# Kernel optimization log

Measured on AMD Instinct MI355X. Metric: run time of the kernel, lower is better.

## Reference

```python
import jax, jax.numpy as jnp
import numpy as np

B, N, D, H = 4, 1024, 256, 8  # batch, seq, in_dim(=per-head qkv_dim), n_heads


def setup_inputs() -> dict:
    key = jax.random.key(0)
    k1, k2, k3 = jax.random.split(key, 3)
    x = jax.random.normal(k1, (B, N, D), dtype=jnp.float32)
    Wqkv = jax.random.normal(k2, (D, 3 * D * H), dtype=jnp.float32) * 0.02
    bqkv = jnp.zeros((3 * D * H,), dtype=jnp.float32)
    W0 = jax.random.normal(k3, (D * H, D), dtype=jnp.float32) * 0.02
    b0 = jnp.zeros((D,), dtype=jnp.float32)
    return {"x": x, "Wqkv": Wqkv, "bqkv": bqkv, "W0": W0, "b0": b0}


def reference(x, Wqkv, bqkv, W0, b0):
    b, n, d = x.shape
    h = Wqkv.shape[1] // (3 * d)
    qkv = x @ Wqkv + bqkv                      # [b, n, 3*d*h]
    # Faithful to torch: raw row-major reinterpretation of the buffer.
    q, k, v = jnp.reshape(qkv, (3, b, n, d, h))
    score = jnp.einsum('bnqh,btqh->bnth', q, k) * (d ** -0.5)  # [b, n, n, h]
    attn = jax.nn.softmax(score, axis=1)       # softmax over query axis (dim=1), as in source
    # einsum 'bnnh,bnqh->bnqh' = diagonal of attn times v (faithful to source)
    av = jnp.einsum('bnnh,bnqh->bnqh', attn, v)  # [b, n, d, h]
    out = av.reshape(b, n, d * h) @ W0 + b0    # [b, n, d]
    return out
```

## Files before the change

### kernel.cpp

```cpp
#include <hip/hip_runtime.h>


#define SEGSZ 8388608

typedef short v8s __attribute__((ext_vector_type(8)));
typedef float v4f __attribute__((ext_vector_type(4)));

__device__ __forceinline__ ushort f2bf(float v) {
  union { float f; unsigned u; } x; x.f = v;
  const unsigned r = x.u + 0x7fff + ((x.u >> 16) & 1);
  return (ushort)(r >> 16);
}
__device__ __forceinline__ float bf2f(ushort v) {
  union { unsigned u; float f; } x; x.u = ((unsigned)v) << 16;
  return x.f;
}

#define GLOAD_LDS16(g, l)                                            \
  __builtin_amdgcn_global_load_lds(                                  \
      (const __attribute__((address_space(1))) void*)(g),            \
      (__attribute__((address_space(3))) void*)(l), 16, 0, 0)

__global__ __launch_bounds__(256) void prep(
    const float* __restrict__ X, const float* __restrict__ Wqkv,
    const float* __restrict__ W0, ushort* __restrict__ xb,
    ushort* __restrict__ whT, ushort* __restrict__ w0T) {
  __shared__ float T[64][65];
  const int tid = threadIdx.x;
  int bid = blockIdx.x;

  if (bid < 1024) {
    const size_t i = ((size_t)bid * 256 + tid) * 4;
    const float4 v = *(const float4*)&X[i];
    ushort4 hv = {f2bf(v.x), f2bf(v.y), f2bf(v.z), f2bf(v.w)};
    *(ushort4*)&xb[i] = hv;
    return;
  }
  bid -= 1024;
  if (bid < 384) {
    const int n0 = (bid % 96) * 64;
    const int k0 = (bid / 96) * 64;
    {
      const int row = tid >> 2;
      const int c0 = (tid & 3) * 16;
#pragma unroll
      for (int j = 0; j < 16; j += 4) {
        const float4 v = *(const float4*)&Wqkv[(size_t)(k0 + row) * 6144 + n0 + c0 + j];
        T[row][c0 + j + 0] = v.x; T[row][c0 + j + 1] = v.y;
        T[row][c0 + j + 2] = v.z; T[row][c0 + j + 3] = v.w;
      }
    }
    __syncthreads();
    {
      const int nn = tid >> 2;
      const int kk0 = (tid & 3) * 16;
      const int n = n0 + nn;
      const int seg = n >> 11, h = n & 7, d = (n & 2047) >> 3;
      const int p = seg * 2048 + h * 256 + d;
      ushort hv[16];
#pragma unroll
      for (int j = 0; j < 16; ++j) hv[j] = f2bf(T[kk0 + j][nn]);
      const size_t base = (size_t)p * 256 + k0 + kk0;
#pragma unroll
      for (int j = 0; j < 16; j += 8) *(v8s*)&whT[base + j] = *(v8s*)&hv[j];
    }
    return;
  }
  bid -= 384;
  {
    const int e0 = (bid & 3) * 64;
    const int k0 = (bid >> 2) * 64;
    {
      const int row = tid >> 2;
      const int c0 = (tid & 3) * 16;
#pragma unroll
      for (int j = 0; j < 16; j += 4) {
        const float4 v = *(const float4*)&W0[(size_t)(k0 + row) * 256 + e0 + c0 + j];
        T[row][c0 + j + 0] = v.x; T[row][c0 + j + 1] = v.y;
        T[row][c0 + j + 2] = v.z; T[row][c0 + j + 3] = v.w;
      }
    }
    __syncthreads();
    {
      const int ee = tid >> 2;
      const int kk0 = (tid & 3) * 16;
#pragma unroll
      for (int j = 0; j < 16; ++j) {
        const int k = k0 + kk0 + j;
        const int d = k >> 3, h = k & 7;
        w0T[(size_t)(e0 + ee) * 2048 + h * 256 + d] = f2bf(T[kk0 + j][ee]);
      }
    }
  }
}

template <int STRIDE>
__device__ __forceinline__ void gemm128_k64(
    const ushort* __restrict__ gA, const ushort* __restrict__ gB,
    ushort (&AS)[8192], ushort (&BS)[8192], v4f (&acc)[4][4]) {
  const int tid = threadIdx.x;
  const int wave = tid >> 6, lane = tid & 63;
  const int quad = lane >> 4, l15 = lane & 15;
  const int wr = (wave >> 1) * 64;
  const int wc = (wave & 1) * 64;
  const int srow = lane >> 3;
  const int scol = (((lane & 7) ^ srow) << 3);

#pragma unroll
  for (int kt = 0; kt < 4; ++kt) {
#pragma unroll
    for (int j = 0; j < 4; ++j) {
      const size_t grow =
          (size_t)(j * 32 + wave * 8 + srow) * STRIDE + kt * 64 + scol;
      GLOAD_LDS16(gA + grow, &AS[j * 2048 + wave * 512]);
      GLOAD_LDS16(gB + grow, &BS[j * 2048 + wave * 512]);
    }
    __syncthreads();
#pragma unroll
    for (int ks = 0; ks < 2; ++ks) {
      v8s aF[4], bF[4];
      const int rx = l15 & 7;
#pragma unroll
      for (int i = 0; i < 4; ++i) {
        aF[i] = *(const v8s*)&AS[(wr + i * 16 + l15) * 64 +
                                 ((((ks << 2) | quad) ^ rx) << 3)];
        bF[i] = *(const v8s*)&BS[(wc + i * 16 + l15) * 64 +
                                 ((((ks << 2) | quad) ^ rx) << 3)];
      }
#pragma unroll
      for (int ri = 0; ri < 4; ++ri)
#pragma unroll
        for (int ci = 0; ci < 4; ++ci)
          acc[ri][ci] = __builtin_amdgcn_mfma_f32_16x16x32_bf16(
              aF[ri], bF[ci], acc[ri][ci], 0, 0, 0);
    }
    __syncthreads();
  }
}

__global__ __launch_bounds__(256) void qkv_mfma(
    const ushort* __restrict__ xb, const ushort* __restrict__ whT,
    const float* __restrict__ bias, ushort* __restrict__ qkvb) {
  __shared__ ushort As[8192];
  __shared__ ushort Bh[8192];
  const int tid = threadIdx.x;
  const int wave = tid >> 6, lane = tid & 63;
  const int quad = lane >> 4, l15 = lane & 15;
  const int c0 = blockIdx.x * 128;
  const int r0 = blockIdx.y * 128;
  const int wr = (wave >> 1) * 64;
  const int wc = (wave & 1) * 64;

  v4f acc[4][4] = {};
  gemm128_k64<256>(xb + (size_t)r0 * 256, whT + (size_t)c0 * 256, As, Bh, acc);

#pragma unroll
  for (int ci = 0; ci < 4; ++ci) {
    const int c = c0 + wc + ci * 16 + l15;
    const int cseg = c >> 11;
    const int h = (c & 2047) >> 8;
    const int d = c & 255;
    const float bv = bias[cseg * 2048 + d * 8 + h];
#pragma unroll
    for (int ri = 0; ri < 4; ++ri)
#pragma unroll
      for (int rg = 0; rg < 4; ++rg) {
        const int r = r0 + wr + ri * 16 + quad * 4 + rg;
        const int g = r * 3 + cseg;
        const int seg = g >> 12;
        const int tok = g & 4095;
        float val = acc[ri][ci][rg] + bv;
        if (seg == 0) val *= 0.0625f;
        qkvb[(size_t)seg * SEGSZ + (size_t)tok * 2048 + h * 256 + d] = f2bf(val);
      }
  }
}

__global__ __launch_bounds__(256) void mid_fused(
    const ushort* __restrict__ qkvb, const ushort* __restrict__ w0T,
    float* __restrict__ pl, float* __restrict__ sd_ws,
    ushort* __restrict__ partial) {
  __shared__ ushort S1[8192];
  __shared__ ushort S2[8192];
  __shared__ float redL[2][2][64];

  const int tid = threadIdx.x;
  const int wave = tid >> 6, lane = tid & 63;
  const int quad = lane >> 4, l15 = lane & 15;
  const int wr = (wave >> 1) * 64;
  const int wc = (wave & 1) * 64;
  const int id = blockIdx.x;

  v4f acc[4][4] = {};

  if (id < 2048) {
    const int bh = (id >> 9) * 8 + (id & 7);
    const int tile = (id >> 3) & 63;
    const int tt0 = (tile >> 3) * 128;
    const int nn0 = (tile & 7) * 128;
    const int b = bh >> 3, h = bh & 7;
    const ushort* Qg = qkvb + (size_t)b * 1024 * 2048 + h * 256;
    const ushort* Kg = Qg + SEGSZ;

    gemm128_k64<2048>(Qg + (size_t)nn0 * 2048, Kg + (size_t)tt0 * 2048,
                      S1, S2, acc);

    float lsum[4];
#pragma unroll
    for (int ci = 0; ci < 4; ++ci) {
      float s = 0.f;
#pragma unroll
      for (int ri = 0; ri < 4; ++ri)
#pragma unroll
        for (int rg = 0; rg < 4; ++rg) s += __expf(acc[ri][ci][rg]);
      s += __shfl_xor(s, 16, 64);
      s += __shfl_xor(s, 32, 64);
      lsum[ci] = s;
    }
    if (quad == 0) {
#pragma unroll
      for (int ci = 0; ci < 4; ++ci)
        redL[wave & 1][wave >> 1][ci * 16 + l15] = lsum[ci];
    }
    __syncthreads();
    if ((wave >> 1) == 0 && quad == 0) {
#pragma unroll
      for (int ci = 0; ci < 4; ++ci) {
        const int t = tt0 + (wave & 1) * 64 + ci * 16 + l15;
        const float l = lsum[ci] + redL[wave & 1][1][ci * 16 + l15];
        pl[((size_t)bh * 1024 + t) * 8 + (tile & 7)] = l;
      }
    }

    if (tt0 == nn0 && (wave == 0 || wave == 3) && quad == (l15 >> 2)) {
#pragma unroll
      for (int ri = 0; ri < 4; ++ri) {
        const int t = tt0 + (wave & 1) * 64 + ri * 16 + l15;
        sd_ws[(size_t)bh * 1024 + t] = acc[ri][ri][l15 & 3];
      }
    }
  } else {
    const int j = id - 2048;
    const int e0 = (j & 1) * 128;
    const int tok0 = ((j >> 1) & 31) * 128;
    const int h = j >> 6;
    const ushort* vb = qkvb + 2 * (size_t)SEGSZ;

    gemm128_k64<2048>(vb + (size_t)tok0 * 2048 + h * 256,
                      w0T + (size_t)e0 * 2048 + h * 256, S1, S2, acc);

#pragma unroll
    for (int ri = 0; ri < 4; ++ri)
#pragma unroll
      for (int rg = 0; rg < 4; ++rg) {
        const int lrow = wr + ri * 16 + quad * 4 + rg;
        const int tok = tok0 + lrow;
#pragma unroll
        for (int ci = 0; ci < 4; ++ci) {
          const int e = e0 + wc + ci * 16 + l15;
          partial[(size_t)h * 1048576 + (size_t)tok * 256 + e] =
              f2bf(acc[ri][ci][rg]);
        }
      }
  }
}

__global__ __launch_bounds__(256) void av_atomic(
    const ushort* __restrict__ vb, const ushort* __restrict__ w0T,
    const float* __restrict__ pl, const float* __restrict__ sd,
    float* __restrict__ out) {
  __shared__ ushort As[8192];
  __shared__ ushort Bs[8192];
  __shared__ float diagS[128];
  const int tid = threadIdx.x;
  const int wave = tid >> 6, lane = tid & 63;
  const int quad = lane >> 4, l15 = lane & 15;
  const int e0 = blockIdx.x * 128;
  const int tok0 = blockIdx.y * 128;
  const int h = blockIdx.z;
  const int wr = (wave >> 1) * 64;
  const int wc = (wave & 1) * 64;

  if (tid < 128) {
    const int bh = (tok0 >> 10) * 8 + h;
    const int t = (tok0 & 1023) + tid;
    const size_t base = ((size_t)bh * 1024 + t) * 8;
    float l = 0.f;
#pragma unroll
    for (int c = 0; c < 8; ++c) l += pl[base + c];
    diagS[tid] = __expf(sd[(size_t)bh * 1024 + t]) / l;
  }
  __syncthreads();

  v4f acc[4][4] = {};
  gemm128_k64<2048>(vb + (size_t)tok0 * 2048 + h * 256,
                    w0T + (size_t)e0 * 2048 + h * 256, As, Bs, acc);

#pragma unroll
  for (int ri = 0; ri < 4; ++ri)
#pragma unroll
    for (int rg = 0; rg < 4; ++rg) {
      const int lrow = wr + ri * 16 + quad * 4 + rg;
      const int tok = tok0 + lrow;
      const float dg = diagS[lrow];
#pragma unroll
      for (int ci = 0; ci < 4; ++ci) {
        const int e = e0 + wc + ci * 16 + l15;
        atomicAdd(&out[(size_t)tok * 256 + e], acc[ri][ci][rg] * dg);
      }
    }
}

__global__ void init_out(const float* __restrict__ b0, float* __restrict__ out) {
  const int i = blockIdx.x * 256 + threadIdx.x;
  const int e0 = (i & 63) << 2;
  *(float4*)&out[(size_t)i * 4] = *(const float4*)&b0[e0];
}

__global__ void reduce_out(const ushort* __restrict__ partial,
                           const float* __restrict__ pl,
                           const float* __restrict__ sd,
                           const float* __restrict__ b0, float* __restrict__ out) {
  __shared__ float dgS[32];
  const int i = blockIdx.x * 256 + threadIdx.x;
  const int tbase = blockIdx.x * 4;
  if (threadIdx.x < 32) {
    const int tl = threadIdx.x >> 3, h = threadIdx.x & 7;
    const int tok = tbase + tl;
    const int bh = (tok >> 10) * 8 + h;
    const int t = tok & 1023;
    const size_t base = ((size_t)bh * 1024 + t) * 8;
    float l = 0.f;
#pragma unroll
    for (int c = 0; c < 8; ++c) l += pl[base + c];
    dgS[threadIdx.x] = __expf(sd[(size_t)bh * 1024 + t]) / l;
  }
  __syncthreads();
  const int tl = threadIdx.x >> 6;
  const int e0 = (i & 63) << 2;
  float4 a = *(const float4*)&b0[e0];
#pragma unroll
  for (int h = 0; h < 8; ++h) {
    const float dg = dgS[tl * 8 + h];
    const ushort4 p = *(const ushort4*)&partial[(size_t)h * 1048576 + (size_t)i * 4];
    a.x += dg * bf2f(p.x); a.y += dg * bf2f(p.y);
    a.z += dg * bf2f(p.z); a.w += dg * bf2f(p.w);
  }
  *(float4*)&out[(size_t)i * 4] = a;
}

extern "C" void kernel_launch(void* const* d_in, const int* in_sizes, int n_in,
                              void* d_out, int out_size, void* d_ws, size_t ws_size,
                              hipStream_t stream) {
  const float* x    = (const float*)d_in[0];
  const float* Wqkv = (const float*)d_in[1];
  const float* bqkv = (const float*)d_in[2];
  const float* W0   = (const float*)d_in[3];
  const float* b0   = (const float*)d_in[4];
  float* out = (float*)d_out;

  float*  pl   = (float*)d_ws;
  float*  sd   = pl + 262144;
  ushort* qkvb = (ushort*)(sd + 32768);
  ushort* xb   = qkvb + 3 * (size_t)SEGSZ;
  ushort* whT  = xb + 1048576;
  ushort* w0T  = whT + 1572864;
  ushort* partial = w0T + 524288;

  ushort* vb = qkvb + 2 * (size_t)SEGSZ;

  const size_t need_base =
      (size_t)(262144 + 32768) * 4 + (size_t)SEGSZ * 3 * 2 +
      (size_t)(1048576 + 1572864 + 524288) * 2;
  const bool full = ws_size >= need_base + (size_t)8 * 1048576 * 2;

  prep<<<1536, 256, 0, stream>>>(x, Wqkv, W0, xb, whT, w0T);
  qkv_mfma<<<dim3(48, 32), 256, 0, stream>>>(xb, whT, bqkv, qkvb);
  if (full) {
    mid_fused<<<2560, 256, 0, stream>>>(qkvb, w0T, pl, sd, partial);
    reduce_out<<<1024, 256, 0, stream>>>(partial, pl, sd, b0, out);
  } else {
    mid_fused<<<2048, 256, 0, stream>>>(qkvb, w0T, pl, sd, nullptr);
    init_out<<<1024, 256, 0, stream>>>(b0, out);
    av_atomic<<<dim3(2, 32, 8), 256, 0, stream>>>(vb, w0T, pl, sd, out);
  }
}
```

Measured before the change: 127.5 us.

## Double-buffer LDS tiles in shared GEMM helper to overlap loads with MFMA

Converts the 128x128xK256 GEMM helper to a two-stage LDS pipeline. It prefetches the next K-slice into the alternate buffer while MFMAs consume the current one, and uses explicit vmcnt waits with raw barriers. The goal is to hide global-to-LDS load latency behind compute. In exchange, LDS use per block doubles to 64KB across all three GEMM kernels, which may lower occupancy.

```diff
diff --git a/kernel.cpp b/kernel.cpp
--- a/kernel.cpp
+++ b/kernel.cpp
@@ -20,6 +20,10 @@
   __builtin_amdgcn_global_load_lds(                                  \
       (const __attribute__((address_space(1))) void*)(g),            \
       (__attribute__((address_space(3))) void*)(l), 16, 0, 0)
+
+#define SBAR()   __builtin_amdgcn_s_barrier()
+#define VMCNT8() asm volatile("s_waitcnt vmcnt(8)" ::: "memory")
+#define VMCNT0() asm volatile("s_waitcnt vmcnt(0)" ::: "memory")
 
 __global__ __launch_bounds__(256) void prep(
     const float* __restrict__ X, const float* __restrict__ Wqkv,
@@ -97,7 +101,7 @@
 template <int STRIDE>
 __device__ __forceinline__ void gemm128_k64(
     const ushort* __restrict__ gA, const ushort* __restrict__ gB,
-    ushort (&AS)[8192], ushort (&BS)[8192], v4f (&acc)[4][4]) {
+    ushort (&AS)[2][8192], ushort (&BS)[2][8192], v4f (&acc)[4][4]) {
   const int tid = threadIdx.x;
   const int wave = tid >> 6, lane = tid & 63;
   const int quad = lane >> 4, l15 = lane & 15;
@@ -106,26 +110,34 @@
   const int srow = lane >> 3;
   const int scol = (((lane & 7) ^ srow) << 3);
 
-#pragma unroll
-  for (int kt = 0; kt < 4; ++kt) {
+  auto stage = [&](int kt, int bi) {
 #pragma unroll
     for (int j = 0; j < 4; ++j) {
       const size_t grow =
           (size_t)(j * 32 + wave * 8 + srow) * STRIDE + kt * 64 + scol;
-      GLOAD_LDS16(gA + grow, &AS[j * 2048 + wave * 512]);
-      GLOAD_LDS16(gB + grow, &BS[j * 2048 + wave * 512]);
-    }
-    __syncthreads();
+      GLOAD_LDS16(gA + grow, &AS[bi][j * 2048 + wave * 512]);
+      GLOAD_LDS16(gB + grow, &BS[bi][j * 2048 + wave * 512]);
+    }
+  };
+
+  stage(0, 0);
+  stage(1, 1);
+  VMCNT8();
+  SBAR();
+
+#pragma unroll
+  for (int kt = 0; kt < 4; ++kt) {
+    const int cur = kt & 1;
 #pragma unroll
     for (int ks = 0; ks < 2; ++ks) {
       v8s aF[4], bF[4];
       const int rx = l15 & 7;
 #pragma unroll
       for (int i = 0; i < 4; ++i) {
-        aF[i] = *(const v8s*)&AS[(wr + i * 16 + l15) * 64 +
-                                 ((((ks << 2) | quad) ^ rx) << 3)];
-        bF[i] = *(const v8s*)&BS[(wc + i * 16 + l15) * 64 +
-                                 ((((ks << 2) | quad) ^ rx) << 3)];
+        aF[i] = *(const v8s*)&AS[cur][(wr + i * 16 + l15) * 64 +
+                                      ((((ks << 2) | quad) ^ rx) << 3)];
+        bF[i] = *(const v8s*)&BS[cur][(wc + i * 16 + l15) * 64 +
+                                      ((((ks << 2) | quad) ^ rx) << 3)];
       }
 #pragma unroll
       for (int ri = 0; ri < 4; ++ri)
@@ -134,15 +146,24 @@
           acc[ri][ci] = __builtin_amdgcn_mfma_f32_16x16x32_bf16(
               aF[ri], bF[ci], acc[ri][ci], 0, 0, 0);
     }
-    __syncthreads();
+    if (kt < 3) {
+      SBAR();
+      if (kt < 2) {
+        stage(kt + 2, cur);
+        VMCNT8();
+      } else {
+        VMCNT0();
+      }
+      SBAR();
+    }
   }
 }
 
 __global__ __launch_bounds__(256) void qkv_mfma(
     const ushort* __restrict__ xb, const ushort* __restrict__ whT,
     const float* __restrict__ bias, ushort* __restrict__ qkvb) {
-  __shared__ ushort As[8192];
-  __shared__ ushort Bh[8192];
+  __shared__ ushort As[2][8192];
+  __shared__ ushort Bh[2][8192];
   const int tid = threadIdx.x;
   const int wave = tid >> 6, lane = tid & 63;
   const int quad = lane >> 4, l15 = lane & 15;
@@ -180,8 +201,8 @@
     const ushort* __restrict__ qkvb, const ushort* __restrict__ w0T,
     float* __restrict__ pl, float* __restrict__ sd_ws,
     ushort* __restrict__ partial) {
-  __shared__ ushort S1[8192];
-  __shared__ ushort S2[8192];
+  __shared__ ushort S1[2][8192];
+  __shared__ ushort S2[2][8192];
   __shared__ float redL[2][2][64];
 
   const int tid = threadIdx.x;
@@ -269,8 +290,8 @@
     const ushort* __restrict__ vb, const ushort* __restrict__ w0T,
     const float* __restrict__ pl, const float* __restrict__ sd,
     float* __restrict__ out) {
-  __shared__ ushort As[8192];
-  __shared__ ushort Bs[8192];
+  __shared__ ushort As[2][8192];
+  __shared__ ushort Bs[2][8192];
   __shared__ float diagS[128];
   const int tid = threadIdx.x;
   const int wave = tid >> 6, lane = tid & 63;
```

After: 128.0 us. Within noise of the previous version (+0.4%).

## Load A operand directly into registers and stage only B through LDS

Applied to the files above, without the earlier changes.

The shared 128x128x256 GEMM helper now loads the A tile fragments straight from global memory into registers and stages only the B tile through LDS. K is processed in two halves of 128 instead of four steps of 64, and the swizzle is widened accordingly. This cuts LDS traffic and the number of barriers per GEMM. In exchange, A fragment loads are uncoalesced strided global reads, and holding 16 A fragments per half raises register pressure, which may lower occupancy.

```diff
diff --git a/kernel.cpp b/kernel.cpp
--- a/kernel.cpp
+++ b/kernel.cpp
@@ -20,6 +20,9 @@
   __builtin_amdgcn_global_load_lds(                                  \
       (const __attribute__((address_space(1))) void*)(g),            \
       (__attribute__((address_space(3))) void*)(l), 16, 0, 0)
+
+#define SBAR()   __builtin_amdgcn_s_barrier()
+#define VMCNT0() asm volatile("s_waitcnt vmcnt(0)" ::: "memory")
 
 __global__ __launch_bounds__(256) void prep(
     const float* __restrict__ X, const float* __restrict__ Wqkv,
@@ -95,54 +98,53 @@
 }
 
 template <int STRIDE>
-__device__ __forceinline__ void gemm128_k64(
+__device__ __forceinline__ void gemm128_breg(
     const ushort* __restrict__ gA, const ushort* __restrict__ gB,
-    ushort (&AS)[8192], ushort (&BS)[8192], v4f (&acc)[4][4]) {
+    ushort (&BS)[16384], v4f (&acc)[4][4]) {
   const int tid = threadIdx.x;
   const int wave = tid >> 6, lane = tid & 63;
   const int quad = lane >> 4, l15 = lane & 15;
   const int wr = (wave >> 1) * 64;
   const int wc = (wave & 1) * 64;
-  const int srow = lane >> 3;
-  const int scol = (((lane & 7) ^ srow) << 3);
-
-#pragma unroll
-  for (int kt = 0; kt < 4; ++kt) {
-#pragma unroll
-    for (int j = 0; j < 4; ++j) {
-      const size_t grow =
-          (size_t)(j * 32 + wave * 8 + srow) * STRIDE + kt * 64 + scol;
-      GLOAD_LDS16(gA + grow, &AS[j * 2048 + wave * 512]);
-      GLOAD_LDS16(gB + grow, &BS[j * 2048 + wave * 512]);
-    }
-    __syncthreads();
-#pragma unroll
-    for (int ks = 0; ks < 2; ++ks) {
-      v8s aF[4], bF[4];
-      const int rx = l15 & 7;
-#pragma unroll
-      for (int i = 0; i < 4; ++i) {
-        aF[i] = *(const v8s*)&AS[(wr + i * 16 + l15) * 64 +
-                                 ((((ks << 2) | quad) ^ rx) << 3)];
-        bF[i] = *(const v8s*)&BS[(wc + i * 16 + l15) * 64 +
-                                 ((((ks << 2) | quad) ^ rx) << 3)];
-      }
-#pragma unroll
-      for (int ri = 0; ri < 4; ++ri)
-#pragma unroll
-        for (int ci = 0; ci < 4; ++ci)
+  const int rlow = tid >> 4;
+  const int srccol = ((l15 ^ rlow) << 3);
+
+#pragma unroll
+  for (int half = 0; half < 2; ++half) {
+    if (half) SBAR();
+    v8s aF[4][4];
+#pragma unroll
+    for (int ri = 0; ri < 4; ++ri)
+#pragma unroll
+      for (int ks = 0; ks < 4; ++ks)
+        aF[ri][ks] = *(const v8s*)&gA[(size_t)(wr + ri * 16 + l15) * STRIDE +
+                                      half * 128 + ks * 32 + quad * 8];
+#pragma unroll
+    for (int j = 0; j < 8; ++j) {
+      GLOAD_LDS16(gB + (size_t)(j * 16 + rlow) * STRIDE + half * 128 + srccol,
+                  &BS[j * 2048 + wave * 512]);
+    }
+    VMCNT0();
+    SBAR();
+#pragma unroll
+    for (int ks = 0; ks < 4; ++ks) {
+#pragma unroll
+      for (int ci = 0; ci < 4; ++ci) {
+        const v8s bF = *(const v8s*)&BS[(wc + ci * 16 + l15) * 128 +
+                                        ((((ks << 2) | quad) ^ l15) << 3)];
+#pragma unroll
+        for (int ri = 0; ri < 4; ++ri)
           acc[ri][ci] = __builtin_amdgcn_mfma_f32_16x16x32_bf16(
-              aF[ri], bF[ci], acc[ri][ci], 0, 0, 0);
-    }
-    __syncthreads();
+              aF[ri][ks], bF, acc[ri][ci], 0, 0, 0);
+      }
+    }
   }
 }
 
 __global__ __launch_bounds__(256) void qkv_mfma(
     const ushort* __restrict__ xb, const ushort* __restrict__ whT,
     const float* __restrict__ bias, ushort* __restrict__ qkvb) {
-  __shared__ ushort As[8192];
-  __shared__ ushort Bh[8192];
+  __shared__ ushort Bs[16384];
   const int tid = threadIdx.x;
   const int wave = tid >> 6, lane = tid & 63;
   const int quad = lane >> 4, l15 = lane & 15;
@@ -152,7 +154,7 @@
   const int wc = (wave & 1) * 64;
 
   v4f acc[4][4] = {};
-  gemm128_k64<256>(xb + (size_t)r0 * 256, whT + (size_t)c0 * 256, As, Bh, acc);
+  gemm128_breg<256>(xb + (size_t)r0 * 256, whT + (size_t)c0 * 256, Bs, acc);
 
 #pragma unroll
   for (int ci = 0; ci < 4; ++ci) {
@@ -180,8 +182,7 @@
     const ushort* __restrict__ qkvb, const ushort* __restrict__ w0T,
     float* __restrict__ pl, float* __restrict__ sd_ws,
     ushort* __restrict__ partial) {
-  __shared__ ushort S1[8192];
-  __shared__ ushort S2[8192];
+  __shared__ ushort Bs[16384];
   __shared__ float redL[2][2][64];
 
   const int tid = threadIdx.x;
@@ -202,8 +203,8 @@
     const ushort* Qg = qkvb + (size_t)b * 1024 * 2048 + h * 256;
     const ushort* Kg = Qg + SEGSZ;
 
-    gemm128_k64<2048>(Qg + (size_t)nn0 * 2048, Kg + (size_t)tt0 * 2048,
-                      S1, S2, acc);
+    gemm128_breg<2048>(Qg + (size_t)nn0 * 2048, Kg + (size_t)tt0 * 2048,
+                       Bs, acc);
 
     float lsum[4];
 #pragma unroll
@@ -246,8 +247,8 @@
     const int h = j >> 6;
     const ushort* vb = qkvb + 2 * (size_t)SEGSZ;
 
-    gemm128_k64<2048>(vb + (size_t)tok0 * 2048 + h * 256,
-                      w0T + (size_t)e0 * 2048 + h * 256, S1, S2, acc);
+    gemm128_breg<2048>(vb + (size_t)tok0 * 2048 + h * 256,
+                       w0T + (size_t)e0 * 2048 + h * 256, Bs, acc);
 
 #pragma unroll
     for (int ri = 0; ri < 4; ++ri)
@@ -269,8 +270,7 @@
     const ushort* __restrict__ vb, const ushort* __restrict__ w0T,
     const float* __restrict__ pl, const float* __restrict__ sd,
     float* __restrict__ out) {
-  __shared__ ushort As[8192];
-  __shared__ ushort Bs[8192];
+  __shared__ ushort Bs[16384];
   __shared__ float diagS[128];
   const int tid = threadIdx.x;
   const int wave = tid >> 6, lane = tid & 63;
@@ -293,8 +293,8 @@
   __syncthreads();
 
   v4f acc[4][4] = {};
-  gemm128_k64<2048>(vb + (size_t)tok0 * 2048 + h * 256,
-                    w0T + (size_t)e0 * 2048 + h * 256, As, Bs, acc);
+  gemm128_breg<2048>(vb + (size_t)tok0 * 2048 + h * 256,
+                     w0T + (size_t)e0 * 2048 + h * 256, Bs, acc);
 
 #pragma unroll
   for (int ri = 0; ri < 4; ++ri)
```

After: 163.5 us. 1.28x slower.

## Store Q/K/V and W0T in contiguous 128x64 tile-blocked layout

Applied to the files above, without the earlier changes.

The QKV projection epilogue and the W0 transpose now write their bf16 outputs in a tiled layout. Each 128-row by 64-column K-slab is a contiguous 16 KB block, grouped per batch-head for Q/K and per head for V. The shared GEMM loader takes separate row and K strides, so the attention and V·W0 GEMMs read each k-tile from one contiguous region instead of rows strided by 2048 elements. The aim is better DRAM and TLB locality on the global-to-LDS loads, at the cost of more scattered, index-heavy stores in the QKV epilogue.

```diff
diff --git a/kernel.cpp b/kernel.cpp
--- a/kernel.cpp
+++ b/kernel.cpp
@@ -84,17 +84,19 @@
     {
       const int ee = tid >> 2;
       const int kk0 = (tid & 3) * 16;
+      const int e = e0 + ee;
 #pragma unroll
       for (int j = 0; j < 16; ++j) {
         const int k = k0 + kk0 + j;
         const int d = k >> 3, h = k & 7;
-        w0T[(size_t)(e0 + ee) * 2048 + h * 256 + d] = f2bf(T[kk0 + j][ee]);
-      }
-    }
-  }
-}
-
-template <int STRIDE>
+        w0T[(size_t)h * 65536 + (e >> 7) * 32768 + (d >> 6) * 8192 +
+            (e & 127) * 64 + (d & 63)] = f2bf(T[kk0 + j][ee]);
+      }
+    }
+  }
+}
+
+template <int RSTRIDE, int KSTRIDE>
 __device__ __forceinline__ void gemm128_k64(
     const ushort* __restrict__ gA, const ushort* __restrict__ gB,
     ushort (&AS)[8192], ushort (&BS)[8192], v4f (&acc)[4][4]) {
@@ -111,7 +113,7 @@
 #pragma unroll
     for (int j = 0; j < 4; ++j) {
       const size_t grow =
-          (size_t)(j * 32 + wave * 8 + srow) * STRIDE + kt * 64 + scol;
+          (size_t)(j * 32 + wave * 8 + srow) * RSTRIDE + kt * KSTRIDE + scol;
       GLOAD_LDS16(gA + grow, &AS[j * 2048 + wave * 512]);
       GLOAD_LDS16(gB + grow, &BS[j * 2048 + wave * 512]);
     }
@@ -152,7 +154,8 @@
   const int wc = (wave & 1) * 64;
 
   v4f acc[4][4] = {};
-  gemm128_k64<256>(xb + (size_t)r0 * 256, whT + (size_t)c0 * 256, As, Bh, acc);
+  gemm128_k64<256, 64>(xb + (size_t)r0 * 256, whT + (size_t)c0 * 256,
+                       As, Bh, acc);
 
 #pragma unroll
   for (int ci = 0; ci < 4; ++ci) {
@@ -171,7 +174,17 @@
         const int tok = g & 4095;
         float val = acc[ri][ci][rg] + bv;
         if (seg == 0) val *= 0.0625f;
-        qkvb[(size_t)seg * SEGSZ + (size_t)tok * 2048 + h * 256 + d] = f2bf(val);
+        size_t addr;
+        if (seg < 2) {
+          const int bh = (tok >> 10) * 8 + h;
+          const int t = tok & 1023;
+          addr = (size_t)seg * SEGSZ + (size_t)bh * 262144 +
+                 (t >> 7) * 32768 + (d >> 6) * 8192 + (t & 127) * 64 + (d & 63);
+        } else {
+          addr = 2 * (size_t)SEGSZ + (size_t)h * 1048576 +
+                 (tok >> 7) * 32768 + (d >> 6) * 8192 + (tok & 127) * 64 + (d & 63);
+        }
+        qkvb[addr] = f2bf(val);
       }
   }
 }
@@ -198,12 +211,10 @@
     const int tile = (id >> 3) & 63;
     const int tt0 = (tile >> 3) * 128;
     const int nn0 = (tile & 7) * 128;
-    const int b = bh >> 3, h = bh & 7;
-    const ushort* Qg = qkvb + (size_t)b * 1024 * 2048 + h * 256;
-    const ushort* Kg = Qg + SEGSZ;
-
-    gemm128_k64<2048>(Qg + (size_t)nn0 * 2048, Kg + (size_t)tt0 * 2048,
-                      S1, S2, acc);
+    const ushort* Qg = qkvb + (size_t)bh * 262144 + (nn0 >> 7) * 32768;
+    const ushort* Kg = qkvb + SEGSZ + (size_t)bh * 262144 + (tt0 >> 7) * 32768;
+
+    gemm128_k64<64, 8192>(Qg, Kg, S1, S2, acc);
 
     float lsum[4];
 #pragma unroll
@@ -244,10 +255,11 @@
     const int e0 = (j & 1) * 128;
     const int tok0 = ((j >> 1) & 31) * 128;
     const int h = j >> 6;
-    const ushort* vb = qkvb + 2 * (size_t)SEGSZ;
-
-    gemm128_k64<2048>(vb + (size_t)tok0 * 2048 + h * 256,
-                      w0T + (size_t)e0 * 2048 + h * 256, S1, S2, acc);
+    const ushort* Ag = qkvb + 2 * (size_t)SEGSZ + (size_t)h * 1048576 +
+                       (tok0 >> 7) * 32768;
+    const ushort* Bg = w0T + (size_t)h * 65536 + (e0 >> 7) * 32768;
+
+    gemm128_k64<64, 8192>(Ag, Bg, S1, S2, acc);
 
 #pragma unroll
     for (int ri = 0; ri < 4; ++ri)
@@ -266,7 +278,7 @@
 }
 
 __global__ __launch_bounds__(256) void av_atomic(
-    const ushort* __restrict__ vb, const ushort* __restrict__ w0T,
+    const ushort* __restrict__ qkvb, const ushort* __restrict__ w0T,
     const float* __restrict__ pl, const float* __restrict__ sd,
     float* __restrict__ out) {
   __shared__ ushort As[8192];
@@ -293,8 +305,10 @@
   __syncthreads();
 
   v4f acc[4][4] = {};
-  gemm128_k64<2048>(vb + (size_t)tok0 * 2048 + h * 256,
-                    w0T + (size_t)e0 * 2048 + h * 256, As, Bs, acc);
+  gemm128_k64<64, 8192>(qkvb + 2 * (size_t)SEGSZ + (size_t)h * 1048576 +
+                            (tok0 >> 7) * 32768,
+                        w0T + (size_t)h * 65536 + (e0 >> 7) * 32768,
+                        As, Bs, acc);
 
 #pragma unroll
   for (int ri = 0; ri < 4; ++ri)
@@ -367,8 +381,6 @@
   ushort* w0T  = whT + 1572864;
   ushort* partial = w0T + 524288;
 
-  ushort* vb = qkvb + 2 * (size_t)SEGSZ;
-
   const size_t need_base =
       (size_t)(262144 + 32768) * 4 + (size_t)SEGSZ * 3 * 2 +
       (size_t)(1048576 + 1572864 + 524288) * 2;
@@ -382,6 +394,6 @@
   } else {
     mid_fused<<<2048, 256, 0, stream>>>(qkvb, w0T, pl, sd, nullptr);
     init_out<<<1024, 256, 0, stream>>>(b0, out);
-    av_atomic<<<dim3(2, 32, 8), 256, 0, stream>>>(vb, w0T, pl, sd, out);
-  }
-}
+    av_atomic<<<dim3(2, 32, 8), 256, 0, stream>>>(qkvb, w0T, pl, sd, out);
+  }
+}
```

Result: slower. 138.9 us (+9.0%).
